# Performance work log

Measured on AMD Instinct MI355X. Metric: run time of the kernel, lower is better.

Reference implementation:

```python
import jax, jax.numpy as jnp
import numpy as np

N = 163842   # icosahedron level-7 vertices
CH = 64
EPS = 1e-5
SLOPE = 0.2

def _bn_lrelu(x, g, b):
    # BatchNorm1d over vertex dim (training-mode batch stats, biased var) + LeakyReLU(0.2)
    mu = jnp.mean(x, axis=0)
    var = jnp.var(x, axis=0)
    y = (x - mu) * jax.lax.rsqrt(var + EPS) * g + b
    return jnp.where(y > 0, y, SLOPE * y)

def _onering_conv(x, neigh, W, bias):
    # gather 7 one-ring neighbors per vertex, flatten, linear project
    n = x.shape[0]
    feat = x[neigh].reshape(n, -1)          # [N, 7*C]
    return feat @ W + bias                  # [N, out]

def setup_inputs() -> dict:
    key = jax.random.key(0)
    ks = jax.random.split(key, 8)
    d = {
        "x": jax.random.normal(ks[0], (N, CH), jnp.float32),
        "neigh_orders": jax.random.randint(ks[1], (7 * N,), 0, N, jnp.int64),
    }
    for i, k in enumerate([1, 2, 3, 4]):
        cin = CH * k
        d[f"g{k}"] = jnp.ones((cin,), jnp.float32)
        d[f"b{k}"] = jnp.zeros((cin,), jnp.float32)
        d[f"W{k}"] = jax.random.normal(ks[2 + i], (7 * cin, CH), jnp.float32) * (1.0 / np.sqrt(7 * cin))
        d[f"wb{k}"] = jnp.zeros((CH,), jnp.float32)
    return d

def reference(x, neigh_orders, g1, b1, g2, b2, g3, b3, g4, b4,
              W1, wb1, W2, wb2, W3, wb3, W4, wb4):
    x1 = _onering_conv(_bn_lrelu(x, g1, b1), neigh_orders, W1, wb1)
    c2 = jnp.concatenate((x, x1), axis=1)
    x2 = _onering_conv(_bn_lrelu(c2, g2, b2), neigh_orders, W2, wb2)
    c3 = jnp.concatenate((x, x1, x2), axis=1)
    x3 = _onering_conv(_bn_lrelu(c3, g3, b3), neigh_orders, W3, wb3)
    c4 = jnp.concatenate((x, x1, x2, x3), axis=1)
    x4 = _onering_conv(_bn_lrelu(c4, g4, b4), neigh_orders, W4, wb4)
    return x4
```

## Files before the change

kernel.cpp:

```cpp
#include <hip/hip_runtime.h>
#include <stdint.h>

#define NV 163842
#define EPSV 1e-5f

using short8 = __attribute__((ext_vector_type(8))) short;
using f32x4  = __attribute__((ext_vector_type(4))) float;

static __device__ __forceinline__ unsigned short f2bf(float f) {
    union { float f; unsigned int i; } v; v.f = f;
    return (unsigned short)((v.i + 0x7FFFu + ((v.i >> 16) & 1u)) >> 16);
}
static __device__ __forceinline__ void bf2x(unsigned int w, float& a, float& b) {
    union { unsigned int i; float f; } lo, hi;
    lo.i = w << 16; hi.i = w & 0xFFFF0000u;
    a = lo.f; b = hi.f;
}
static __device__ __forceinline__ unsigned int pack2(float a, float b) {
    union { float f; unsigned int i; } ua, ub; ua.f = a; ub.f = b;
    return __builtin_amdgcn_perm(ub.i + 0x8000u, ua.i + 0x8000u, 0x07060302);
}

static __device__ __forceinline__ void gl_lds16(const unsigned short* g, unsigned short* l) {
    __builtin_amdgcn_global_load_lds((__attribute__((address_space(1))) void*)g,
                                     (__attribute__((address_space(3))) void*)l, 16, 0, 0);
}

__global__ __launch_bounds__(256) void k_zero(float* __restrict__ ACC) {
    ACC[threadIdx.x] = 0.f;
    ACC[256 + threadIdx.x] = 0.f;
}

__global__ __launch_bounds__(256) void k_cast(const float* __restrict__ x,
                                              unsigned short* __restrict__ C,
                                              float* __restrict__ ACC) {
    const int t = threadIdx.x;
    const int wv = t >> 6, lane = t & 63;
    const int v = blockIdx.x * 64 + (t >> 2);
    const int c0 = (t & 3) * 16;
    float f[16];
    const bool valid = v < NV;
    if (valid) {
        const float4* p = (const float4*)(x + (size_t)v * 64 + c0);
#pragma unroll
        for (int i = 0; i < 4; ++i) {
            float4 q = p[i];
            f[i * 4 + 0] = q.x; f[i * 4 + 1] = q.y; f[i * 4 + 2] = q.z; f[i * 4 + 3] = q.w;
        }
        unsigned int o[8];
#pragma unroll
        for (int i = 0; i < 8; ++i)
            o[i] = ((unsigned int)f2bf(f[2 * i])) | (((unsigned int)f2bf(f[2 * i + 1])) << 16);
        uint4* dst = (uint4*)(C + (size_t)v * 256 + c0);
        dst[0] = uint4{o[0], o[1], o[2], o[3]};
        dst[1] = uint4{o[4], o[5], o[6], o[7]};
    } else {
#pragma unroll
        for (int i = 0; i < 16; ++i) f[i] = 0.f;
    }
    float s[16], s2[16];
#pragma unroll
    for (int i = 0; i < 16; ++i) { s[i] = f[i]; s2[i] = f[i] * f[i]; }
#pragma unroll
    for (int mask = 4; mask <= 32; mask <<= 1) {
#pragma unroll
        for (int i = 0; i < 16; ++i) {
            s[i]  += __shfl_xor(s[i],  mask);
            s2[i] += __shfl_xor(s2[i], mask);
        }
    }
    __shared__ float red[4 * 128];
    if ((lane >> 2) == 0) {
        int cb = (lane & 3) * 16;
#pragma unroll
        for (int i = 0; i < 16; ++i) {
            red[wv * 128 + cb + i]      = s[i];
            red[wv * 128 + 64 + cb + i] = s2[i];
        }
    }
    __syncthreads();
    if (t < 128) {
        float v4 = red[t] + red[128 + t] + red[256 + t] + red[384 + t];
        int c = t & 63, which = t >> 6;
        atomicAdd(&ACC[which * 256 + c], v4);
    }
}

__global__ __launch_bounds__(256) void k_wt_all(const float* __restrict__ W1,
                                                const float* __restrict__ W2,
                                                const float* __restrict__ W3,
                                                const float* __restrict__ W4,
                                                unsigned short* __restrict__ WT) {
    int j = blockIdx.x * 256 + threadIdx.x;
    if (j >= 286720) return;
    const float* W; int jj, K7;
    if (j < 28672)       { W = W1; jj = j;          K7 = 448;  }
    else if (j < 86016)  { W = W2; jj = j - 28672;  K7 = 896;  }
    else if (j < 172032) { W = W3; jj = j - 86016;  K7 = 1344; }
    else                 { W = W4; jj = j - 172032; K7 = 1792; }
    int n = jj / K7, k = jj - n * K7;
    WT[j] = f2bf(W[(size_t)k * 64 + n]);
}

template<int CIN>
__global__ __launch_bounds__(256) void k_norm(const unsigned short* __restrict__ C,
                                              const float* __restrict__ ACC,
                                              const float* __restrict__ g,
                                              const float* __restrict__ b,
                                              unsigned short* __restrict__ CN) {
    __shared__ float ssc[256], ssh[256];
    const int t = threadIdx.x;
    if (t < CIN) {
        float s = ACC[t], s2 = ACC[256 + t];
        float mu = s * (1.0f / NV);
        float var = fmaf(-mu, mu, s2 * (1.0f / NV));
        float sc = g[t] * rsqrtf(var + EPSV);
        ssc[t] = sc;
        ssh[t] = b[t] - mu * sc;
    }
    __syncthreads();
    constexpr int C8 = CIN / 8;
    const int total = NV * C8;
    for (int idx = blockIdx.x * 256 + t; idx < total; idx += gridDim.x * 256) {
        int v = idx / C8;
        int c8 = idx - v * C8;
        int ch = c8 * 8;
        uint4 u = *(const uint4*)(C + (size_t)v * 256 + ch);
        unsigned int in[4] = {u.x, u.y, u.z, u.w}, o[4];
#pragma unroll
        for (int j = 0; j < 4; ++j) {
            float lo, hi; bf2x(in[j], lo, hi);
            float y0 = fmaf(lo, ssc[ch + 2 * j],     ssh[ch + 2 * j]);
            float y1 = fmaf(hi, ssc[ch + 2 * j + 1], ssh[ch + 2 * j + 1]);
            y0 = y0 > 0.f ? y0 : 0.2f * y0;
            y1 = y1 > 0.f ? y1 : 0.2f * y1;
            o[j] = pack2(y0, y1);
        }
        *(uint4*)(CN + (size_t)v * CIN + ch) = uint4{o[0], o[1], o[2], o[3]};
    }
}

template<int CIN, int GRP, bool FINAL>
__global__ __launch_bounds__(256) void k_gg(const unsigned short* __restrict__ CN,
                                            const int* __restrict__ neigh,
                                            const unsigned short* __restrict__ WT,
                                            const float* __restrict__ wb,
                                            float* __restrict__ ACC,
                                            unsigned short* __restrict__ Cout,
                                            float* __restrict__ Fout) {
    constexpr int KB = CIN / 64;
    constexpr int NC = 7 * KB;
    constexpr int K7 = 7 * CIN;

    __shared__ int sIdx[896];
    __shared__ unsigned short sA[2][128 * 64];
    __shared__ unsigned short sW[2][64 * 64];

    const int t = threadIdx.x;
    const int v0 = blockIdx.x * 128;
    const int wv = t >> 6, lane = t & 63;
    const int m = lane & 15, quad = lane >> 4;
    const int rowin = lane >> 3, slot = lane & 7;
    const int sw = ((slot ^ rowin) * 8);

    for (int q = t; q < 896; q += 256) {
        int gi = v0 * 7 + q;
        sIdx[q] = (gi < NV * 7) ? neigh[gi] : 0;
    }

    f32x4 acc[2][4];
#pragma unroll
    for (int i = 0; i < 2; ++i)
#pragma unroll
        for (int j = 0; j < 4; ++j) acc[i][j] = f32x4{0.f, 0.f, 0.f, 0.f};

    __syncthreads();

    auto issue_stage = [&](int r, int kb, int c, int b) {
#pragma unroll
        for (int i = 0; i < 4; ++i) {
            int gidx = sIdx[(wv * 32 + i * 8 + rowin) * 7 + r];
            gl_lds16(CN + (size_t)gidx * CIN + kb * 64 + sw, &sA[b][(wv * 32 + i * 8) * 64]);
        }
#pragma unroll
        for (int j = 0; j < 2; ++j) {
            int n = wv * 16 + j * 8 + rowin;
            gl_lds16(WT + (size_t)n * K7 + c * 64 + sw, &sW[b][(wv * 16 + j * 8) * 64]);
        }
    };
    auto compute = [&](int b) {
        __builtin_amdgcn_s_setprio(1);
#pragma unroll
        for (int s = 0; s < 2; ++s) {
            const int sx = ((s * 4 + quad) ^ (m & 7)) * 8;
            short8 af0 = *(const short8*)(&sA[b][(wv * 32 + m) * 64 + sx]);
            short8 af1 = *(const short8*)(&sA[b][(wv * 32 + 16 + m) * 64 + sx]);
#pragma unroll
            for (int ct = 0; ct < 4; ++ct) {
                short8 bf = *(const short8*)(&sW[b][(ct * 16 + m) * 64 + sx]);
                acc[0][ct] = __builtin_amdgcn_mfma_f32_16x16x32_bf16(af0, bf, acc[0][ct], 0, 0, 0);
                acc[1][ct] = __builtin_amdgcn_mfma_f32_16x16x32_bf16(af1, bf, acc[1][ct], 0, 0, 0);
            }
        }
        __builtin_amdgcn_s_setprio(0);
    };

    issue_stage(0, 0, 0, 0);
    __syncthreads();

    int r = 0, kb = 0, buf = 0;
    for (int c = 0; c < NC - 1; ++c) {
        int kb1 = kb + 1, r1 = r;
        if (kb1 == KB) { kb1 = 0; r1 = r + 1; }
        issue_stage(r1, kb1, c + 1, buf ^ 1);
        compute(buf);
        __syncthreads();
        r = r1; kb = kb1; buf ^= 1;
    }
    compute(buf);
    __syncthreads();

    float bsum[4]  = {0.f, 0.f, 0.f, 0.f};
    float b2sum[4] = {0.f, 0.f, 0.f, 0.f};
#pragma unroll
    for (int mt = 0; mt < 2; ++mt) {
#pragma unroll
        for (int ct = 0; ct < 4; ++ct) {
            int col = ct * 16 + m;
            float bv = wb[col];
#pragma unroll
            for (int j = 0; j < 4; ++j) {
                int vr = v0 + wv * 32 + mt * 16 + quad * 4 + j;
                float val = acc[mt][ct][j] + bv;
                if (vr < NV) {
                    if (FINAL) {
                        Fout[(size_t)vr * 64 + col] = val;
                    } else {
                        Cout[(size_t)vr * 256 + GRP * 64 + col] = f2bf(val);
                        bsum[ct] += val; b2sum[ct] += val * val;
                    }
                }
            }
        }
    }
    if (!FINAL) {
#pragma unroll
        for (int ct = 0; ct < 4; ++ct) {
            bsum[ct]  += __shfl_xor(bsum[ct], 16);
            bsum[ct]  += __shfl_xor(bsum[ct], 32);
            b2sum[ct] += __shfl_xor(b2sum[ct], 16);
            b2sum[ct] += __shfl_xor(b2sum[ct], 32);
        }
        float* red = (float*)&sA[0][0];
        if (quad == 0) {
#pragma unroll
            for (int ct = 0; ct < 4; ++ct) {
                red[wv * 128 + ct * 16 + m]       = bsum[ct];
                red[512 + wv * 128 + ct * 16 + m] = b2sum[ct];
            }
        }
        __syncthreads();
        if (t < 128) {
            int c = t & 63, which = t >> 6;
            float v = red[which * 512 + c] + red[which * 512 + 128 + c] +
                      red[which * 512 + 256 + c] + red[which * 512 + 384 + c];
            atomicAdd(&ACC[which * 256 + GRP * 64 + c], v);
        }
    }
}

extern "C" void kernel_launch(void* const* d_in, const int* in_sizes, int n_in,
                              void* d_out, int out_size, void* d_ws, size_t ws_size,
                              hipStream_t stream) {
    const float* x     = (const float*)d_in[0];
    const int*   neigh = (const int*)d_in[1];
    const float* G[4]  = {(const float*)d_in[2],  (const float*)d_in[6],
                          (const float*)d_in[10], (const float*)d_in[14]};
    const float* B[4]  = {(const float*)d_in[3],  (const float*)d_in[7],
                          (const float*)d_in[11], (const float*)d_in[15]};
    const float* W[4]  = {(const float*)d_in[4],  (const float*)d_in[8],
                          (const float*)d_in[12], (const float*)d_in[16]};
    const float* WB[4] = {(const float*)d_in[5],  (const float*)d_in[9],
                          (const float*)d_in[13], (const float*)d_in[17]};
    float* out = (float*)d_out;

    char* ws = (char*)d_ws;
    size_t off = 0;
    unsigned short* C  = (unsigned short*)(ws + off); off += (size_t)NV * 256 * 2;
    unsigned short* CN = (unsigned short*)(ws + off); off += (size_t)NV * 256 * 2;
    unsigned short* WT = (unsigned short*)(ws + off); off += (size_t)286720 * 2;
    float* ACC         = (float*)(ws + off);          off += 512 * 4;

    k_zero<<<1, 256, 0, stream>>>(ACC);
    k_cast<<<(NV + 63) / 64, 256, 0, stream>>>(x, C, ACC);
    k_wt_all<<<(286720 + 255) / 256, 256, 0, stream>>>(W[0], W[1], W[2], W[3], WT);

    const int GG = (NV + 127) / 128;
    const int NB = 2048;

    k_norm< 64><<<NB, 256, 0, stream>>>(C, ACC, G[0], B[0], CN);
    k_gg< 64, 1, false><<<GG, 256, 0, stream>>>(CN, neigh, WT,          WB[0], ACC, C, nullptr);
    k_norm<128><<<NB, 256, 0, stream>>>(C, ACC, G[1], B[1], CN);
    k_gg<128, 2, false><<<GG, 256, 0, stream>>>(CN, neigh, WT + 28672,  WB[1], ACC, C, nullptr);
    k_norm<192><<<NB, 256, 0, stream>>>(C, ACC, G[2], B[2], CN);
    k_gg<192, 3, false><<<GG, 256, 0, stream>>>(CN, neigh, WT + 86016,  WB[2], ACC, C, nullptr);
    k_norm<256><<<NB, 256, 0, stream>>>(C, ACC, G[3], B[3], CN);
    k_gg<256, 0, true ><<<GG, 256, 0, stream>>>(CN, neigh, WT + 172032, WB[3], ACC, nullptr, out);
}
```

Before: 554.6 us.

## Load weight fragments into registers and drop per-chunk block barriers

The weight tile no longer goes through shared memory. Each lane now loads its MFMA B fragments straight from global memory into registers, double-buffered one chunk ahead. The neighbor-gathered A tile still goes to LDS, but each wave only touches its own rows, so the per-iteration __syncthreads is replaced by explicit vmcnt waits and the loop is fully unrolled. This is meant to remove LDS traffic and block-wide barrier stalls, at the cost of more VGPRs, larger code, redundant weight reads from cache across blocks, and reliance on wave-local ordering for reuse of the LDS buffers.

```diff
diff --git a/kernel.cpp b/kernel.cpp
--- a/kernel.cpp
+++ b/kernel.cpp
@@ -154,7 +154,6 @@
 
     __shared__ int sIdx[896];
     __shared__ unsigned short sA[2][128 * 64];
-    __shared__ unsigned short sW[2][64 * 64];
 
     const int t = threadIdx.x;
     const int v0 = blockIdx.x * 128;
@@ -176,48 +175,56 @@
 
     __syncthreads();
 
-    auto issue_stage = [&](int r, int kb, int c, int b) {
+    auto stageA = [&](int c) {
+        int r = c / KB, kb = c - r * KB;
 #pragma unroll
         for (int i = 0; i < 4; ++i) {
             int gidx = sIdx[(wv * 32 + i * 8 + rowin) * 7 + r];
-            gl_lds16(CN + (size_t)gidx * CIN + kb * 64 + sw, &sA[b][(wv * 32 + i * 8) * 64]);
-        }
-#pragma unroll
-        for (int j = 0; j < 2; ++j) {
-            int n = wv * 16 + j * 8 + rowin;
-            gl_lds16(WT + (size_t)n * K7 + c * 64 + sw, &sW[b][(wv * 16 + j * 8) * 64]);
+            gl_lds16(CN + (size_t)gidx * CIN + kb * 64 + sw, &sA[c & 1][(wv * 32 + i * 8) * 64]);
         }
     };
-    auto compute = [&](int b) {
+    auto loadB = [&](int c, short8 (&b)[4][2]) {
+#pragma unroll
+        for (int ct = 0; ct < 4; ++ct) {
+            const unsigned short* wp = WT + (size_t)(ct * 16 + m) * K7 + c * 64 + quad * 8;
+            b[ct][0] = *(const short8*)(wp);
+            b[ct][1] = *(const short8*)(wp + 32);
+        }
+    };
+    auto step = [&](int c, short8 (&bc)[4][2], short8 (&bn)[4][2]) {
+        if (c + 1 < NC) {
+            loadB(c + 1, bn);
+            stageA(c + 1);
+            asm volatile("s_waitcnt vmcnt(12)" ::: "memory");
+        } else {
+            asm volatile("s_waitcnt vmcnt(0)" ::: "memory");
+        }
+        __builtin_amdgcn_sched_barrier(0);
+        const unsigned short* sa = &sA[c & 1][0];
         __builtin_amdgcn_s_setprio(1);
 #pragma unroll
         for (int s = 0; s < 2; ++s) {
             const int sx = ((s * 4 + quad) ^ (m & 7)) * 8;
-            short8 af0 = *(const short8*)(&sA[b][(wv * 32 + m) * 64 + sx]);
-            short8 af1 = *(const short8*)(&sA[b][(wv * 32 + 16 + m) * 64 + sx]);
+            short8 af0 = *(const short8*)(sa + (wv * 32 + m) * 64 + sx);
+            short8 af1 = *(const short8*)(sa + (wv * 32 + 16 + m) * 64 + sx);
 #pragma unroll
             for (int ct = 0; ct < 4; ++ct) {
-                short8 bf = *(const short8*)(&sW[b][(ct * 16 + m) * 64 + sx]);
-                acc[0][ct] = __builtin_amdgcn_mfma_f32_16x16x32_bf16(af0, bf, acc[0][ct], 0, 0, 0);
-                acc[1][ct] = __builtin_amdgcn_mfma_f32_16x16x32_bf16(af1, bf, acc[1][ct], 0, 0, 0);
+                acc[0][ct] = __builtin_amdgcn_mfma_f32_16x16x32_bf16(af0, bc[ct][s], acc[0][ct], 0, 0, 0);
+                acc[1][ct] = __builtin_amdgcn_mfma_f32_16x16x32_bf16(af1, bc[ct][s], acc[1][ct], 0, 0, 0);
             }
         }
         __builtin_amdgcn_s_setprio(0);
     };
 
-    issue_stage(0, 0, 0, 0);
-    __syncthreads();
-
-    int r = 0, kb = 0, buf = 0;
-    for (int c = 0; c < NC - 1; ++c) {
-        int kb1 = kb + 1, r1 = r;
-        if (kb1 == KB) { kb1 = 0; r1 = r + 1; }
-        issue_stage(r1, kb1, c + 1, buf ^ 1);
-        compute(buf);
-        __syncthreads();
-        r = r1; kb = kb1; buf ^= 1;
-    }
-    compute(buf);
+    short8 b0[4][2], b1[4][2];
+    loadB(0, b0);
+    stageA(0);
+#pragma unroll
+    for (int c = 0; c < NC; ++c) {
+        if (c & 1) step(c, b1, b0);
+        else       step(c, b0, b1);
+    }
+
     __syncthreads();
 
     float bsum[4]  = {0.f, 0.f, 0.f, 0.f};
```

Measured after the change: 723.1 us. 30.4% more time.

## Skip re-normalizing channel groups whose BN params match earlier layers; fuse cast and weight prep

Applied to the files above, without the earlier changes.

The normalized buffer CN now uses a fixed 256-channel row stride. Each norm pass checks at runtime whether a 64-channel group's gamma/beta slice matches the layer that last wrote it. Because batch stats for earlier channels do not change, a matching group can reuse the CN values already stored and skip its normalization pass. The cast and weight-transpose kernels are merged into one launch, and the accumulator zeroing kernel is replaced by a memset. The payoff depends on identical BN parameters across layers, which holds for the test inputs. The per-thread parameter comparison adds a small cost per block.

```diff
diff --git a/kernel.cpp b/kernel.cpp
--- a/kernel.cpp
+++ b/kernel.cpp
@@ -26,15 +26,29 @@
                                      (__attribute__((address_space(3))) void*)l, 16, 0, 0);
 }
 
-__global__ __launch_bounds__(256) void k_zero(float* __restrict__ ACC) {
-    ACC[threadIdx.x] = 0.f;
-    ACC[256 + threadIdx.x] = 0.f;
-}
-
-__global__ __launch_bounds__(256) void k_cast(const float* __restrict__ x,
-                                              unsigned short* __restrict__ C,
-                                              float* __restrict__ ACC) {
+#define CAST_BLOCKS 2561
+#define WT_BLOCKS   1120
+__global__ __launch_bounds__(256) void k_cast_wt(const float* __restrict__ x,
+                                                 unsigned short* __restrict__ C,
+                                                 float* __restrict__ ACC,
+                                                 const float* __restrict__ W1,
+                                                 const float* __restrict__ W2,
+                                                 const float* __restrict__ W3,
+                                                 const float* __restrict__ W4,
+                                                 unsigned short* __restrict__ WT) {
     const int t = threadIdx.x;
+    if (blockIdx.x >= CAST_BLOCKS) {
+        int j = (blockIdx.x - CAST_BLOCKS) * 256 + t;
+        if (j >= 286720) return;
+        const float* W; int jj, K7;
+        if (j < 28672)       { W = W1; jj = j;          K7 = 448;  }
+        else if (j < 86016)  { W = W2; jj = j - 28672;  K7 = 896;  }
+        else if (j < 172032) { W = W3; jj = j - 86016;  K7 = 1344; }
+        else                 { W = W4; jj = j - 172032; K7 = 1792; }
+        int n = jj / K7, k = jj - n * K7;
+        WT[j] = f2bf(W[(size_t)k * 64 + n]);
+        return;
+    }
     const int wv = t >> 6, lane = t & 63;
     const int v = blockIdx.x * 64 + (t >> 2);
     const int c0 = (t & 3) * 16;
@@ -86,57 +100,64 @@
     }
 }
 
-__global__ __launch_bounds__(256) void k_wt_all(const float* __restrict__ W1,
-                                                const float* __restrict__ W2,
-                                                const float* __restrict__ W3,
-                                                const float* __restrict__ W4,
-                                                unsigned short* __restrict__ WT) {
-    int j = blockIdx.x * 256 + threadIdx.x;
-    if (j >= 286720) return;
-    const float* W; int jj, K7;
-    if (j < 28672)       { W = W1; jj = j;          K7 = 448;  }
-    else if (j < 86016)  { W = W2; jj = j - 28672;  K7 = 896;  }
-    else if (j < 172032) { W = W3; jj = j - 86016;  K7 = 1344; }
-    else                 { W = W4; jj = j - 172032; K7 = 1792; }
-    int n = jj / K7, k = jj - n * K7;
-    WT[j] = f2bf(W[(size_t)k * 64 + n]);
-}
-
-template<int CIN>
+template<int L>
 __global__ __launch_bounds__(256) void k_norm(const unsigned short* __restrict__ C,
                                               const float* __restrict__ ACC,
-                                              const float* __restrict__ g,
-                                              const float* __restrict__ b,
+                                              const float* __restrict__ G1, const float* __restrict__ B1,
+                                              const float* __restrict__ G2, const float* __restrict__ B2,
+                                              const float* __restrict__ G3, const float* __restrict__ B3,
+                                              const float* __restrict__ G4, const float* __restrict__ B4,
                                               unsigned short* __restrict__ CN) {
+    constexpr int CIN = 64 * L;
     __shared__ float ssc[256], ssh[256];
     const int t = threadIdx.x;
+    const float* Gs[4] = {G1, G2, G3, G4};
+    const float* Bs[4] = {B1, B2, B3, B4};
     if (t < CIN) {
         float s = ACC[t], s2 = ACC[256 + t];
         float mu = s * (1.0f / NV);
         float var = fmaf(-mu, mu, s2 * (1.0f / NV));
-        float sc = g[t] * rsqrtf(var + EPSV);
+        float sc = Gs[L - 1][t] * rsqrtf(var + EPSV);
         ssc[t] = sc;
-        ssh[t] = b[t] - mu * sc;
-    }
-    __syncthreads();
-    constexpr int C8 = CIN / 8;
-    const int total = NV * C8;
-    for (int idx = blockIdx.x * 256 + t; idx < total; idx += gridDim.x * 256) {
-        int v = idx / C8;
-        int c8 = idx - v * C8;
-        int ch = c8 * 8;
-        uint4 u = *(const uint4*)(C + (size_t)v * 256 + ch);
-        unsigned int in[4] = {u.x, u.y, u.z, u.w}, o[4];
-#pragma unroll
-        for (int j = 0; j < 4; ++j) {
-            float lo, hi; bf2x(in[j], lo, hi);
-            float y0 = fmaf(lo, ssc[ch + 2 * j],     ssh[ch + 2 * j]);
-            float y1 = fmaf(hi, ssc[ch + 2 * j + 1], ssh[ch + 2 * j + 1]);
-            y0 = y0 > 0.f ? y0 : 0.2f * y0;
-            y1 = y1 > 0.f ? y1 : 0.2f * y1;
-            o[j] = pack2(y0, y1);
-        }
-        *(uint4*)(CN + (size_t)v * CIN + ch) = uint4{o[0], o[1], o[2], o[3]};
+        ssh[t] = Bs[L - 1][t] - mu * sc;
+    }
+    __syncthreads();
+
+    auto differs = [&](const float* ga, const float* ba,
+                       const float* gb, const float* bb, int off) -> bool {
+        for (int c = 0; c < 64; ++c)
+            if (ga[off + c] != gb[off + c] || ba[off + c] != bb[off + c]) return true;
+        return false;
+    };
+
+    for (int g = 0; g < L; ++g) {
+        bool need;
+        if (g == L - 1) {
+            need = true;
+        } else {
+            int effL = g;
+            for (int l = g + 1; l <= L - 2; ++l)
+                if (differs(Gs[l], Bs[l], Gs[effL], Bs[effL], g * 64)) effL = l;
+            need = differs(Gs[L - 1], Bs[L - 1], Gs[effL], Bs[effL], g * 64);
+        }
+        if (!need) continue;
+        const int total = NV * 8;
+        for (int idx = blockIdx.x * 256 + t; idx < total; idx += gridDim.x * 256) {
+            int v = idx >> 3;
+            int ch = g * 64 + (idx & 7) * 8;
+            uint4 u = *(const uint4*)(C + (size_t)v * 256 + ch);
+            unsigned int in[4] = {u.x, u.y, u.z, u.w}, o[4];
+#pragma unroll
+            for (int j = 0; j < 4; ++j) {
+                float lo, hi; bf2x(in[j], lo, hi);
+                float y0 = fmaf(lo, ssc[ch + 2 * j],     ssh[ch + 2 * j]);
+                float y1 = fmaf(hi, ssc[ch + 2 * j + 1], ssh[ch + 2 * j + 1]);
+                y0 = y0 > 0.f ? y0 : 0.2f * y0;
+                y1 = y1 > 0.f ? y1 : 0.2f * y1;
+                o[j] = pack2(y0, y1);
+            }
+            *(uint4*)(CN + (size_t)v * 256 + ch) = uint4{o[0], o[1], o[2], o[3]};
+        }
     }
 }
 
@@ -180,7 +201,7 @@
 #pragma unroll
         for (int i = 0; i < 4; ++i) {
             int gidx = sIdx[(wv * 32 + i * 8 + rowin) * 7 + r];
-            gl_lds16(CN + (size_t)gidx * CIN + kb * 64 + sw, &sA[b][(wv * 32 + i * 8) * 64]);
+            gl_lds16(CN + (size_t)gidx * 256 + kb * 64 + sw, &sA[b][(wv * 32 + i * 8) * 64]);
         }
 #pragma unroll
         for (int j = 0; j < 2; ++j) {
@@ -291,19 +312,19 @@
     unsigned short* WT = (unsigned short*)(ws + off); off += (size_t)286720 * 2;
     float* ACC         = (float*)(ws + off);          off += 512 * 4;
 
-    k_zero<<<1, 256, 0, stream>>>(ACC);
-    k_cast<<<(NV + 63) / 64, 256, 0, stream>>>(x, C, ACC);
-    k_wt_all<<<(286720 + 255) / 256, 256, 0, stream>>>(W[0], W[1], W[2], W[3], WT);
+    hipMemsetAsync(ACC, 0, 512 * sizeof(float), stream);
+    k_cast_wt<<<CAST_BLOCKS + WT_BLOCKS, 256, 0, stream>>>(x, C, ACC,
+                                                           W[0], W[1], W[2], W[3], WT);
 
     const int GG = (NV + 127) / 128;
     const int NB = 2048;
 
-    k_norm< 64><<<NB, 256, 0, stream>>>(C, ACC, G[0], B[0], CN);
+    k_norm<1><<<NB, 256, 0, stream>>>(C, ACC, G[0], B[0], G[1], B[1], G[2], B[2], G[3], B[3], CN);
     k_gg< 64, 1, false><<<GG, 256, 0, stream>>>(CN, neigh, WT,          WB[0], ACC, C, nullptr);
-    k_norm<128><<<NB, 256, 0, stream>>>(C, ACC, G[1], B[1], CN);
+    k_norm<2><<<NB, 256, 0, stream>>>(C, ACC, G[0], B[0], G[1], B[1], G[2], B[2], G[3], B[3], CN);
     k_gg<128, 2, false><<<GG, 256, 0, stream>>>(CN, neigh, WT + 28672,  WB[1], ACC, C, nullptr);
-    k_norm<192><<<NB, 256, 0, stream>>>(C, ACC, G[2], B[2], CN);
+    k_norm<3><<<NB, 256, 0, stream>>>(C, ACC, G[0], B[0], G[1], B[1], G[2], B[2], G[3], B[3], CN);
     k_gg<192, 3, false><<<GG, 256, 0, stream>>>(CN, neigh, WT + 86016,  WB[2], ACC, C, nullptr);
-    k_norm<256><<<NB, 256, 0, stream>>>(C, ACC, G[3], B[3], CN);
+    k_norm<4><<<NB, 256, 0, stream>>>(C, ACC, G[0], B[0], G[1], B[1], G[2], B[2], G[3], B[3], CN);
     k_gg<256, 0, true ><<<GG, 256, 0, stream>>>(CN, neigh, WT + 172032, WB[3], ACC, nullptr, out);
 }
```

Result: slower. 676.4 us (+22.0%).

## Fuse all stages into persistent megakernel with grid barriers and incremental BN

Applied to the files above, without the earlier changes.

Replaces the chain of separate cast, weight-transpose, norm and gather-GEMM launches with one persistent kernel of 512 blocks. The stages are separated by a software grid barrier built on atomics. The normalized buffer now keeps a fixed 256-channel stride, so a channel group only has to be re-normalized when its gamma or beta differ from the previous layer's, which is checked at runtime. This removes launch gaps and redundant normalization traffic. In exchange it relies on all blocks being co-resident for the spin barrier. Distributing 1281 tiles over 512 blocks may also leave an uneven tail and lower occupancy than the original full-grid GEMM launches.

```diff
diff --git a/kernel.cpp b/kernel.cpp
--- a/kernel.cpp
+++ b/kernel.cpp
@@ -2,7 +2,9 @@
 #include <stdint.h>
 
 #define NV 163842
+#define NTILE 1281
 #define EPSV 1e-5f
+#define GRID_BLOCKS 512
 
 using short8 = __attribute__((ext_vector_type(8))) short;
 using f32x4  = __attribute__((ext_vector_type(4))) float;
@@ -20,290 +22,323 @@
     union { float f; unsigned int i; } ua, ub; ua.f = a; ub.f = b;
     return __builtin_amdgcn_perm(ub.i + 0x8000u, ua.i + 0x8000u, 0x07060302);
 }
-
 static __device__ __forceinline__ void gl_lds16(const unsigned short* g, unsigned short* l) {
     __builtin_amdgcn_global_load_lds((__attribute__((address_space(1))) void*)g,
                                      (__attribute__((address_space(3))) void*)l, 16, 0, 0);
 }
 
-__global__ __launch_bounds__(256) void k_zero(float* __restrict__ ACC) {
-    ACC[threadIdx.x] = 0.f;
-    ACC[256 + threadIdx.x] = 0.f;
-}
-
-__global__ __launch_bounds__(256) void k_cast(const float* __restrict__ x,
-                                              unsigned short* __restrict__ C,
-                                              float* __restrict__ ACC) {
+static __device__ __forceinline__ void gridBarrier(unsigned int* BAR) {
+    __threadfence();
+    __syncthreads();
+    if (threadIdx.x == 0) {
+        unsigned int* cnt = BAR;
+        unsigned int* gen = BAR + 1;
+        unsigned int g = atomicAdd(gen, 0u);
+        if (atomicAdd(cnt, 1u) == (unsigned)gridDim.x - 1u) {
+            atomicExch(cnt, 0u);
+            atomicAdd(gen, 1u);
+        } else {
+            int guard = 0;
+            while (atomicAdd(gen, 0u) == g) {
+                __builtin_amdgcn_s_sleep(32);
+                if (++guard > 300000) break;
+            }
+        }
+    }
+    __syncthreads();
+    __threadfence();
+}
+
+struct MegaArgs {
+    const float* x; const int* neigh;
+    const float* G[4]; const float* B[4]; const float* W[4]; const float* WB[4];
+    float* out;
+    unsigned short* C; unsigned short* CN; unsigned short* WT; float* ACC;
+    unsigned int* BAR;
+};
+
+static __device__ __forceinline__ void norm_phase(unsigned char* smem, int L,
+                                                  const MegaArgs& a) {
+    float* ssc = (float*)smem;
+    float* ssh = ssc + 256;
     const int t = threadIdx.x;
-    const int wv = t >> 6, lane = t & 63;
-    const int v = blockIdx.x * 64 + (t >> 2);
-    const int c0 = (t & 3) * 16;
-    float f[16];
-    const bool valid = v < NV;
-    if (valid) {
-        const float4* p = (const float4*)(x + (size_t)v * 64 + c0);
-#pragma unroll
-        for (int i = 0; i < 4; ++i) {
-            float4 q = p[i];
-            f[i * 4 + 0] = q.x; f[i * 4 + 1] = q.y; f[i * 4 + 2] = q.z; f[i * 4 + 3] = q.w;
-        }
-        unsigned int o[8];
-#pragma unroll
-        for (int i = 0; i < 8; ++i)
-            o[i] = ((unsigned int)f2bf(f[2 * i])) | (((unsigned int)f2bf(f[2 * i + 1])) << 16);
-        uint4* dst = (uint4*)(C + (size_t)v * 256 + c0);
-        dst[0] = uint4{o[0], o[1], o[2], o[3]};
-        dst[1] = uint4{o[4], o[5], o[6], o[7]};
-    } else {
-#pragma unroll
-        for (int i = 0; i < 16; ++i) f[i] = 0.f;
-    }
-    float s[16], s2[16];
-#pragma unroll
-    for (int i = 0; i < 16; ++i) { s[i] = f[i]; s2[i] = f[i] * f[i]; }
-#pragma unroll
-    for (int mask = 4; mask <= 32; mask <<= 1) {
-#pragma unroll
-        for (int i = 0; i < 16; ++i) {
-            s[i]  += __shfl_xor(s[i],  mask);
-            s2[i] += __shfl_xor(s2[i], mask);
-        }
-    }
-    __shared__ float red[4 * 128];
-    if ((lane >> 2) == 0) {
-        int cb = (lane & 3) * 16;
-#pragma unroll
-        for (int i = 0; i < 16; ++i) {
-            red[wv * 128 + cb + i]      = s[i];
-            red[wv * 128 + 64 + cb + i] = s2[i];
-        }
-    }
-    __syncthreads();
-    if (t < 128) {
-        float v4 = red[t] + red[128 + t] + red[256 + t] + red[384 + t];
-        int c = t & 63, which = t >> 6;
-        atomicAdd(&ACC[which * 256 + c], v4);
-    }
-}
-
-__global__ __launch_bounds__(256) void k_wt_all(const float* __restrict__ W1,
-                                                const float* __restrict__ W2,
-                                                const float* __restrict__ W3,
-                                                const float* __restrict__ W4,
-                                                unsigned short* __restrict__ WT) {
-    int j = blockIdx.x * 256 + threadIdx.x;
-    if (j >= 286720) return;
-    const float* W; int jj, K7;
-    if (j < 28672)       { W = W1; jj = j;          K7 = 448;  }
-    else if (j < 86016)  { W = W2; jj = j - 28672;  K7 = 896;  }
-    else if (j < 172032) { W = W3; jj = j - 86016;  K7 = 1344; }
-    else                 { W = W4; jj = j - 172032; K7 = 1792; }
-    int n = jj / K7, k = jj - n * K7;
-    WT[j] = f2bf(W[(size_t)k * 64 + n]);
-}
-
-template<int CIN>
-__global__ __launch_bounds__(256) void k_norm(const unsigned short* __restrict__ C,
-                                              const float* __restrict__ ACC,
-                                              const float* __restrict__ g,
-                                              const float* __restrict__ b,
-                                              unsigned short* __restrict__ CN) {
-    __shared__ float ssc[256], ssh[256];
-    const int t = threadIdx.x;
+    const int CIN = 64 * L;
     if (t < CIN) {
-        float s = ACC[t], s2 = ACC[256 + t];
+        float s = a.ACC[t], s2 = a.ACC[256 + t];
         float mu = s * (1.0f / NV);
         float var = fmaf(-mu, mu, s2 * (1.0f / NV));
-        float sc = g[t] * rsqrtf(var + EPSV);
+        float sc = a.G[L - 1][t] * rsqrtf(var + EPSV);
         ssc[t] = sc;
-        ssh[t] = b[t] - mu * sc;
+        ssh[t] = a.B[L - 1][t] - mu * sc;
     }
     __syncthreads();
-    constexpr int C8 = CIN / 8;
-    const int total = NV * C8;
-    for (int idx = blockIdx.x * 256 + t; idx < total; idx += gridDim.x * 256) {
-        int v = idx / C8;
-        int c8 = idx - v * C8;
-        int ch = c8 * 8;
-        uint4 u = *(const uint4*)(C + (size_t)v * 256 + ch);
-        unsigned int in[4] = {u.x, u.y, u.z, u.w}, o[4];
-#pragma unroll
-        for (int j = 0; j < 4; ++j) {
-            float lo, hi; bf2x(in[j], lo, hi);
-            float y0 = fmaf(lo, ssc[ch + 2 * j],     ssh[ch + 2 * j]);
-            float y1 = fmaf(hi, ssc[ch + 2 * j + 1], ssh[ch + 2 * j + 1]);
-            y0 = y0 > 0.f ? y0 : 0.2f * y0;
-            y1 = y1 > 0.f ? y1 : 0.2f * y1;
-            o[j] = pack2(y0, y1);
-        }
-        *(uint4*)(CN + (size_t)v * CIN + ch) = uint4{o[0], o[1], o[2], o[3]};
+    const int lc = t & 63;
+    for (int grp = 0; grp < L; ++grp) {
+        bool need;
+        if (grp == L - 1) {
+            need = true;
+        } else {
+            int effL = grp;
+            for (int l = grp + 1; l <= L - 2; ++l) {
+                int c = grp * 64 + lc;
+                bool d = (a.G[l][c] != a.G[effL][c]) || (a.B[l][c] != a.B[effL][c]);
+                if (__any(d)) effL = l;
+            }
+            int c = grp * 64 + lc;
+            bool d = (a.G[L - 1][c] != a.G[effL][c]) || (a.B[L - 1][c] != a.B[effL][c]);
+            need = __any(d);
+        }
+        if (!need) continue;
+        const int total = NV * 8;
+        for (int idx = blockIdx.x * 256 + t; idx < total; idx += gridDim.x * 256) {
+            int v = idx >> 3;
+            int ch = grp * 64 + (idx & 7) * 8;
+            uint4 u = *(const uint4*)(a.C + (size_t)v * 256 + ch);
+            unsigned int in[4] = {u.x, u.y, u.z, u.w}, o[4];
+#pragma unroll
+            for (int j = 0; j < 4; ++j) {
+                float lo, hi; bf2x(in[j], lo, hi);
+                float y0 = fmaf(lo, ssc[ch + 2 * j],     ssh[ch + 2 * j]);
+                float y1 = fmaf(hi, ssc[ch + 2 * j + 1], ssh[ch + 2 * j + 1]);
+                y0 = y0 > 0.f ? y0 : 0.2f * y0;
+                y1 = y1 > 0.f ? y1 : 0.2f * y1;
+                o[j] = pack2(y0, y1);
+            }
+            *(uint4*)(a.CN + (size_t)v * 256 + ch) = uint4{o[0], o[1], o[2], o[3]};
+        }
     }
 }
 
 template<int CIN, int GRP, bool FINAL>
-__global__ __launch_bounds__(256) void k_gg(const unsigned short* __restrict__ CN,
-                                            const int* __restrict__ neigh,
-                                            const unsigned short* __restrict__ WT,
-                                            const float* __restrict__ wb,
-                                            float* __restrict__ ACC,
-                                            unsigned short* __restrict__ Cout,
-                                            float* __restrict__ Fout) {
+static __device__ __forceinline__ void gg_phase(unsigned char* smem, const MegaArgs& a,
+                                                const unsigned short* WTl,
+                                                const float* wb) {
     constexpr int KB = CIN / 64;
     constexpr int NC = 7 * KB;
     constexpr int K7 = 7 * CIN;
-
-    __shared__ int sIdx[896];
-    __shared__ unsigned short sA[2][128 * 64];
-    __shared__ unsigned short sW[2][64 * 64];
+    int* sIdx = (int*)smem;
+    auto sA = (unsigned short (*)[128 * 64])(smem + 3584);
+    auto sW = (unsigned short (*)[64 * 64])(smem + 3584 + 32768);
 
     const int t = threadIdx.x;
-    const int v0 = blockIdx.x * 128;
     const int wv = t >> 6, lane = t & 63;
     const int m = lane & 15, quad = lane >> 4;
     const int rowin = lane >> 3, slot = lane & 7;
     const int sw = ((slot ^ rowin) * 8);
 
-    for (int q = t; q < 896; q += 256) {
-        int gi = v0 * 7 + q;
-        sIdx[q] = (gi < NV * 7) ? neigh[gi] : 0;
-    }
-
-    f32x4 acc[2][4];
-#pragma unroll
-    for (int i = 0; i < 2; ++i)
-#pragma unroll
-        for (int j = 0; j < 4; ++j) acc[i][j] = f32x4{0.f, 0.f, 0.f, 0.f};
-
-    __syncthreads();
-
-    auto issue_stage = [&](int r, int kb, int c, int b) {
-#pragma unroll
-        for (int i = 0; i < 4; ++i) {
-            int gidx = sIdx[(wv * 32 + i * 8 + rowin) * 7 + r];
-            gl_lds16(CN + (size_t)gidx * CIN + kb * 64 + sw, &sA[b][(wv * 32 + i * 8) * 64]);
-        }
-#pragma unroll
-        for (int j = 0; j < 2; ++j) {
-            int n = wv * 16 + j * 8 + rowin;
-            gl_lds16(WT + (size_t)n * K7 + c * 64 + sw, &sW[b][(wv * 16 + j * 8) * 64]);
-        }
-    };
-    auto compute = [&](int b) {
-        __builtin_amdgcn_s_setprio(1);
-#pragma unroll
-        for (int s = 0; s < 2; ++s) {
-            const int sx = ((s * 4 + quad) ^ (m & 7)) * 8;
-            short8 af0 = *(const short8*)(&sA[b][(wv * 32 + m) * 64 + sx]);
-            short8 af1 = *(const short8*)(&sA[b][(wv * 32 + 16 + m) * 64 + sx]);
-#pragma unroll
-            for (int ct = 0; ct < 4; ++ct) {
-                short8 bf = *(const short8*)(&sW[b][(ct * 16 + m) * 64 + sx]);
-                acc[0][ct] = __builtin_amdgcn_mfma_f32_16x16x32_bf16(af0, bf, acc[0][ct], 0, 0, 0);
-                acc[1][ct] = __builtin_amdgcn_mfma_f32_16x16x32_bf16(af1, bf, acc[1][ct], 0, 0, 0);
-            }
-        }
-        __builtin_amdgcn_s_setprio(0);
-    };
-
-    issue_stage(0, 0, 0, 0);
-    __syncthreads();
-
-    int r = 0, kb = 0, buf = 0;
-    for (int c = 0; c < NC - 1; ++c) {
-        int kb1 = kb + 1, r1 = r;
-        if (kb1 == KB) { kb1 = 0; r1 = r + 1; }
-        issue_stage(r1, kb1, c + 1, buf ^ 1);
+    for (int tile = blockIdx.x; tile < NTILE; tile += gridDim.x) {
+        const int v0 = tile * 128;
+        for (int q = t; q < 896; q += 256) {
+            int gi = v0 * 7 + q;
+            sIdx[q] = (gi < NV * 7) ? a.neigh[gi] : 0;
+        }
+        f32x4 acc[2][4];
+#pragma unroll
+        for (int i = 0; i < 2; ++i)
+#pragma unroll
+            for (int j = 0; j < 4; ++j) acc[i][j] = f32x4{0.f, 0.f, 0.f, 0.f};
+        __syncthreads();
+
+        auto issue_stage = [&](int r, int kb, int c, int b) {
+#pragma unroll
+            for (int i = 0; i < 4; ++i) {
+                int gidx = sIdx[(wv * 32 + i * 8 + rowin) * 7 + r];
+                gl_lds16(a.CN + (size_t)gidx * 256 + kb * 64 + sw, &sA[b][(wv * 32 + i * 8) * 64]);
+            }
+#pragma unroll
+            for (int j = 0; j < 2; ++j) {
+                int n = wv * 16 + j * 8 + rowin;
+                gl_lds16(WTl + (size_t)n * K7 + c * 64 + sw, &sW[b][(wv * 16 + j * 8) * 64]);
+            }
+        };
+        auto compute = [&](int b) {
+            __builtin_amdgcn_s_setprio(1);
+#pragma unroll
+            for (int s = 0; s < 2; ++s) {
+                const int sx = ((s * 4 + quad) ^ (m & 7)) * 8;
+                short8 af0 = *(const short8*)(&sA[b][(wv * 32 + m) * 64 + sx]);
+                short8 af1 = *(const short8*)(&sA[b][(wv * 32 + 16 + m) * 64 + sx]);
+#pragma unroll
+                for (int ct = 0; ct < 4; ++ct) {
+                    short8 bf = *(const short8*)(&sW[b][(ct * 16 + m) * 64 + sx]);
+                    acc[0][ct] = __builtin_amdgcn_mfma_f32_16x16x32_bf16(af0, bf, acc[0][ct], 0, 0, 0);
+                    acc[1][ct] = __builtin_amdgcn_mfma_f32_16x16x32_bf16(af1, bf, acc[1][ct], 0, 0, 0);
+                }
+            }
+            __builtin_amdgcn_s_setprio(0);
+        };
+
+        issue_stage(0, 0, 0, 0);
+        __syncthreads();
+        int r = 0, kb = 0, buf = 0;
+        for (int c = 0; c < NC - 1; ++c) {
+            int kb1 = kb + 1, r1 = r;
+            if (kb1 == KB) { kb1 = 0; r1 = r + 1; }
+            issue_stage(r1, kb1, c + 1, buf ^ 1);
+            compute(buf);
+            __syncthreads();
+            r = r1; kb = kb1; buf ^= 1;
+        }
         compute(buf);
         __syncthreads();
-        r = r1; kb = kb1; buf ^= 1;
-    }
-    compute(buf);
-    __syncthreads();
-
-    float bsum[4]  = {0.f, 0.f, 0.f, 0.f};
-    float b2sum[4] = {0.f, 0.f, 0.f, 0.f};
-#pragma unroll
-    for (int mt = 0; mt < 2; ++mt) {
-#pragma unroll
-        for (int ct = 0; ct < 4; ++ct) {
-            int col = ct * 16 + m;
-            float bv = wb[col];
-#pragma unroll
-            for (int j = 0; j < 4; ++j) {
-                int vr = v0 + wv * 32 + mt * 16 + quad * 4 + j;
-                float val = acc[mt][ct][j] + bv;
-                if (vr < NV) {
-                    if (FINAL) {
-                        Fout[(size_t)vr * 64 + col] = val;
-                    } else {
-                        Cout[(size_t)vr * 256 + GRP * 64 + col] = f2bf(val);
-                        bsum[ct] += val; b2sum[ct] += val * val;
+
+        float bsum[4]  = {0.f, 0.f, 0.f, 0.f};
+        float b2sum[4] = {0.f, 0.f, 0.f, 0.f};
+#pragma unroll
+        for (int mt = 0; mt < 2; ++mt) {
+#pragma unroll
+            for (int ct = 0; ct < 4; ++ct) {
+                int col = ct * 16 + m;
+                float bv = wb[col];
+#pragma unroll
+                for (int j = 0; j < 4; ++j) {
+                    int vr = v0 + wv * 32 + mt * 16 + quad * 4 + j;
+                    float val = acc[mt][ct][j] + bv;
+                    if (vr < NV) {
+                        if (FINAL) {
+                            a.out[(size_t)vr * 64 + col] = val;
+                        } else {
+                            a.C[(size_t)vr * 256 + GRP * 64 + col] = f2bf(val);
+                            bsum[ct] += val; b2sum[ct] += val * val;
+                        }
                     }
                 }
             }
         }
-    }
-    if (!FINAL) {
-#pragma unroll
-        for (int ct = 0; ct < 4; ++ct) {
-            bsum[ct]  += __shfl_xor(bsum[ct], 16);
-            bsum[ct]  += __shfl_xor(bsum[ct], 32);
-            b2sum[ct] += __shfl_xor(b2sum[ct], 16);
-            b2sum[ct] += __shfl_xor(b2sum[ct], 32);
-        }
-        float* red = (float*)&sA[0][0];
-        if (quad == 0) {
+        if (!FINAL) {
 #pragma unroll
             for (int ct = 0; ct < 4; ++ct) {
-                red[wv * 128 + ct * 16 + m]       = bsum[ct];
-                red[512 + wv * 128 + ct * 16 + m] = b2sum[ct];
-            }
-        }
-        __syncthreads();
-        if (t < 128) {
-            int c = t & 63, which = t >> 6;
-            float v = red[which * 512 + c] + red[which * 512 + 128 + c] +
-                      red[which * 512 + 256 + c] + red[which * 512 + 384 + c];
-            atomicAdd(&ACC[which * 256 + GRP * 64 + c], v);
-        }
-    }
+                bsum[ct]  += __shfl_xor(bsum[ct], 16);
+                bsum[ct]  += __shfl_xor(bsum[ct], 32);
+                b2sum[ct] += __shfl_xor(b2sum[ct], 16);
+                b2sum[ct] += __shfl_xor(b2sum[ct], 32);
+            }
+            float* red = (float*)&sA[0][0];
+            if (quad == 0) {
+#pragma unroll
+                for (int ct = 0; ct < 4; ++ct) {
+                    red[wv * 128 + ct * 16 + m]       = bsum[ct];
+                    red[512 + wv * 128 + ct * 16 + m] = b2sum[ct];
+                }
+            }
+            __syncthreads();
+            if (t < 128) {
+                int c = t & 63, which = t >> 6;
+                float v = red[which * 512 + c] + red[which * 512 + 128 + c] +
+                          red[which * 512 + 256 + c] + red[which * 512 + 384 + c];
+                atomicAdd(&a.ACC[which * 256 + GRP * 64 + c], v);
+            }
+        }
+    }
+}
+
+__global__ __launch_bounds__(256, 2) void k_mega(MegaArgs a) {
+    __shared__ __align__(16) unsigned char smem[52736];
+    const int t = threadIdx.x;
+
+    for (int j = blockIdx.x * 256 + t; j < 286720; j += gridDim.x * 256) {
+        const float* W; int jj, K7;
+        if (j < 28672)       { W = a.W[0]; jj = j;          K7 = 448;  }
+        else if (j < 86016)  { W = a.W[1]; jj = j - 28672;  K7 = 896;  }
+        else if (j < 172032) { W = a.W[2]; jj = j - 86016;  K7 = 1344; }
+        else                 { W = a.W[3]; jj = j - 172032; K7 = 1792; }
+        int n = jj / K7, k = jj - n * K7;
+        a.WT[j] = f2bf(W[(size_t)k * 64 + n]);
+    }
+    {
+        float* red = (float*)smem;
+        const int wv = t >> 6, lane = t & 63;
+        float statAcc = 0.f;
+        for (int vb = blockIdx.x; vb < 2561; vb += gridDim.x) {
+            const int v = vb * 64 + (t >> 2);
+            const int c0 = (t & 3) * 16;
+            float f[16];
+            const bool valid = v < NV;
+            if (valid) {
+                const float4* p = (const float4*)(a.x + (size_t)v * 64 + c0);
+#pragma unroll
+                for (int i = 0; i < 4; ++i) {
+                    float4 q = p[i];
+                    f[i * 4 + 0] = q.x; f[i * 4 + 1] = q.y; f[i * 4 + 2] = q.z; f[i * 4 + 3] = q.w;
+                }
+                unsigned int o[8];
+#pragma unroll
+                for (int i = 0; i < 8; ++i)
+                    o[i] = ((unsigned int)f2bf(f[2 * i])) | (((unsigned int)f2bf(f[2 * i + 1])) << 16);
+                uint4* dst = (uint4*)(a.C + (size_t)v * 256 + c0);
+                dst[0] = uint4{o[0], o[1], o[2], o[3]};
+                dst[1] = uint4{o[4], o[5], o[6], o[7]};
+            } else {
+#pragma unroll
+                for (int i = 0; i < 16; ++i) f[i] = 0.f;
+            }
+            float s[16], s2[16];
+#pragma unroll
+            for (int i = 0; i < 16; ++i) { s[i] = f[i]; s2[i] = f[i] * f[i]; }
+#pragma unroll
+            for (int mask = 4; mask <= 32; mask <<= 1) {
+#pragma unroll
+                for (int i = 0; i < 16; ++i) {
+                    s[i]  += __shfl_xor(s[i],  mask);
+                    s2[i] += __shfl_xor(s2[i], mask);
+                }
+            }
+            if ((lane >> 2) == 0) {
+                int cb = (lane & 3) * 16;
+#pragma unroll
+                for (int i = 0; i < 16; ++i) {
+                    red[wv * 128 + cb + i]      = s[i];
+                    red[wv * 128 + 64 + cb + i] = s2[i];
+                }
+            }
+            __syncthreads();
+            if (t < 128) statAcc += red[t] + red[128 + t] + red[256 + t] + red[384 + t];
+            __syncthreads();
+        }
+        if (t < 128) atomicAdd(&a.ACC[(t >> 6) * 256 + (t & 63)], statAcc);
+    }
+    gridBarrier(a.BAR);
+
+    norm_phase(smem, 1, a);
+    gridBarrier(a.BAR);
+    gg_phase< 64, 1, false>(smem, a, a.WT,          a.WB[0]);
+    gridBarrier(a.BAR);
+    norm_phase(smem, 2, a);
+    gridBarrier(a.BAR);
+    gg_phase<128, 2, false>(smem, a, a.WT + 28672,  a.WB[1]);
+    gridBarrier(a.BAR);
+    norm_phase(smem, 3, a);
+    gridBarrier(a.BAR);
+    gg_phase<192, 3, false>(smem, a, a.WT + 86016,  a.WB[2]);
+    gridBarrier(a.BAR);
+    norm_phase(smem, 4, a);
+    gridBarrier(a.BAR);
+    gg_phase<256, 0, true >(smem, a, a.WT + 172032, a.WB[3]);
 }
 
 extern "C" void kernel_launch(void* const* d_in, const int* in_sizes, int n_in,
                               void* d_out, int out_size, void* d_ws, size_t ws_size,
                               hipStream_t stream) {
-    const float* x     = (const float*)d_in[0];
-    const int*   neigh = (const int*)d_in[1];
-    const float* G[4]  = {(const float*)d_in[2],  (const float*)d_in[6],
-                          (const float*)d_in[10], (const float*)d_in[14]};
-    const float* B[4]  = {(const float*)d_in[3],  (const float*)d_in[7],
-                          (const float*)d_in[11], (const float*)d_in[15]};
-    const float* W[4]  = {(const float*)d_in[4],  (const float*)d_in[8],
-                          (const float*)d_in[12], (const float*)d_in[16]};
-    const float* WB[4] = {(const float*)d_in[5],  (const float*)d_in[9],
-                          (const float*)d_in[13], (const float*)d_in[17]};
-    float* out = (float*)d_out;
-
     char* ws = (char*)d_ws;
     size_t off = 0;
     unsigned short* C  = (unsigned short*)(ws + off); off += (size_t)NV * 256 * 2;
     unsigned short* CN = (unsigned short*)(ws + off); off += (size_t)NV * 256 * 2;
     unsigned short* WT = (unsigned short*)(ws + off); off += (size_t)286720 * 2;
     float* ACC         = (float*)(ws + off);          off += 512 * 4;
-
-    k_zero<<<1, 256, 0, stream>>>(ACC);
-    k_cast<<<(NV + 63) / 64, 256, 0, stream>>>(x, C, ACC);
-    k_wt_all<<<(286720 + 255) / 256, 256, 0, stream>>>(W[0], W[1], W[2], W[3], WT);
-
-    const int GG = (NV + 127) / 128;
-    const int NB = 2048;
-
-    k_norm< 64><<<NB, 256, 0, stream>>>(C, ACC, G[0], B[0], CN);
-    k_gg< 64, 1, false><<<GG, 256, 0, stream>>>(CN, neigh, WT,          WB[0], ACC, C, nullptr);
-    k_norm<128><<<NB, 256, 0, stream>>>(C, ACC, G[1], B[1], CN);
-    k_gg<128, 2, false><<<GG, 256, 0, stream>>>(CN, neigh, WT + 28672,  WB[1], ACC, C, nullptr);
-    k_norm<192><<<NB, 256, 0, stream>>>(C, ACC, G[2], B[2], CN);
-    k_gg<192, 3, false><<<GG, 256, 0, stream>>>(CN, neigh, WT + 86016,  WB[2], ACC, C, nullptr);
-    k_norm<256><<<NB, 256, 0, stream>>>(C, ACC, G[3], B[3], CN);
-    k_gg<256, 0, true ><<<GG, 256, 0, stream>>>(CN, neigh, WT + 172032, WB[3], ACC, nullptr, out);
-}
+    unsigned int* BAR  = (unsigned int*)(ws + off);   off += 64;
+
+    MegaArgs ma;
+    ma.x     = (const float*)d_in[0];
+    ma.neigh = (const int*)d_in[1];
+    for (int i = 0; i < 4; ++i) {
+        ma.G[i]  = (const float*)d_in[2 + 4 * i];
+        ma.B[i]  = (const float*)d_in[3 + 4 * i];
+        ma.W[i]  = (const float*)d_in[4 + 4 * i];
+        ma.WB[i] = (const float*)d_in[5 + 4 * i];
+    }
+    ma.out = (float*)d_out;
+    ma.C = C; ma.CN = CN; ma.WT = WT; ma.ACC = ACC; ma.BAR = BAR;
+
+    hipMemsetAsync(ACC, 0, 512 * sizeof(float) + 64, stream);
+    k_mega<<<GRID_BLOCKS, 256, 0, stream>>>(ma);
+}
```

Measured after the change: 1.335 ms. 2.41x slower.
